# Optimization experiments

Hardware: AMD Instinct MI355X
Metric: run time of the kernel (lower is better)

Reference implementation:

```python
import jax, jax.numpy as jnp
import numpy as np

N_NODES = 50000
N_EDGES = 800000
D_IN = 128
D_HID = 128
NUM_LAYERS = 3
NUM_GRAPHS = 50


def setup_inputs() -> dict:
    key = jax.random.key(0)
    ks = jax.random.split(key, 8)
    x = jax.random.normal(ks[0], (N_NODES, D_IN), dtype=jnp.float32)
    edge_index = jax.random.randint(ks[1], (2, N_EDGES), 0, N_NODES, dtype=jnp.int32)
    batch = jnp.sort(jax.random.randint(ks[2], (N_NODES,), 0, NUM_GRAPHS, dtype=jnp.int32))
    # glorot-ish init for GCN weights and fc weights
    scale = 1.0 / np.sqrt(D_HID)
    Wc = jax.random.normal(ks[3], (NUM_LAYERS, D_IN, D_HID), dtype=jnp.float32) * scale
    bc = jnp.zeros((NUM_LAYERS, D_HID), dtype=jnp.float32)
    Wf = jax.random.normal(ks[4], (NUM_LAYERS, D_HID, D_HID), dtype=jnp.float32) * scale
    bf = jnp.zeros((NUM_LAYERS, D_HID), dtype=jnp.float32)
    return {"x": x, "edge_index": edge_index, "batch": batch,
            "Wc": Wc, "bc": bc, "Wf": Wf, "bf": bf}


def _gcn_forward(x, Wc, bc, Wf, bf, src, dst, deg_inv_sqrt, batch):
    norm = deg_inv_sqrt[src] * deg_inv_sqrt[dst]  # [E+N]
    for i in range(NUM_LAYERS):
        h = x @ Wc[i]                              # [N, D_HID] linear transform
        msg = h[src] * norm[:, None]               # gather + normalize, [E+N, D_HID]
        x = jax.ops.segment_sum(msg, dst, num_segments=N_NODES) + bc[i]
        x = jax.nn.relu(x)
    x = jax.ops.segment_sum(x, batch, num_segments=NUM_GRAPHS)  # global_add_pool
    for i in range(NUM_LAYERS):
        x = jax.nn.relu(x @ Wf[i] + bf[i])
    return x  # [NUM_GRAPHS, D_HID]


def reference(x, edge_index, batch, Wc, bc, Wf, bf):
    # add self-loops (PyG GCNConv default) and compute symmetric normalization
    loops = jnp.arange(N_NODES, dtype=edge_index.dtype)
    src = jnp.concatenate([edge_index[0], loops])
    dst = jnp.concatenate([edge_index[1], loops])
    deg = jax.ops.segment_sum(jnp.ones_like(dst, dtype=x.dtype), dst,
                              num_segments=N_NODES)
    deg_inv_sqrt = jnp.where(deg > 0, jax.lax.rsqrt(jnp.maximum(deg, 1.0)), 0.0)
    return _gcn_forward(x, Wc, bc, Wf, bf, src, dst, deg_inv_sqrt, batch)
```

## Files before the change

kernel.cpp:

```cpp
#include <hip/hip_runtime.h>

#define N_NODES 50000
#define N_EDGES 800000
#define D 128
#define NGRAPH 50

typedef unsigned int uint32;
typedef unsigned short u16;
typedef __attribute__((ext_vector_type(8))) short short8;
typedef __attribute__((ext_vector_type(4))) float f32x4;

__device__ inline float bf_lo(uint32 u) { union { uint32 u; float f; } c; c.u = u << 16; return c.f; }
__device__ inline float bf_hi(uint32 u) { union { uint32 u; float f; } c; c.u = u & 0xffff0000u; return c.f; }
__device__ inline u16 f2bf(float f) {
  union { float f; uint32 u; } c; c.f = f;
  uint32 r = (c.u + 0x7fffu + ((c.u >> 16) & 1u)) >> 16;
  return (u16)r;
}

__global__ void k_init(int* __restrict__ deg, const float* __restrict__ Wc,
                       u16* __restrict__ WT, const int* __restrict__ batch,
                       int* __restrict__ gstart) {
  int i = blockIdx.x * 256 + threadIdx.x;
  if (i < N_NODES) deg[i] = 0;
  if (i < 3 * 128 * 128) {
    int layer = i >> 14, rem = i & 16383;
    int n = rem >> 7, k = rem & 127;
    WT[i] = f2bf(Wc[layer * 16384 + k * 128 + n]);
  }
  if (i <= NGRAPH) {
    int lo = 0, hi = N_NODES;
    while (lo < hi) {
      int mid = (lo + hi) >> 1;
      if (batch[mid] < i) lo = mid + 1; else hi = mid;
    }
    gstart[i] = lo;
  }
}

__global__ void k_degfill(const int* __restrict__ src, const int* __restrict__ dst,
                          int* __restrict__ deg, u16* __restrict__ csr) {
  int part = blockIdx.x & 7;
  int e = (blockIdx.x >> 3) * 256 + threadIdx.x;
  if (e < N_EDGES) {
    int d = dst[e];
    if (d / 6250 == part) {
      int r = atomicAdd(&deg[d], 1);
      csr[(d << 6) + r] = (u16)src[e];
    }
  }
}

__global__ void k_prescale(const float4* __restrict__ x, const int* __restrict__ deg,
                           uint4* __restrict__ xs) {
  int i = blockIdx.x * 256 + threadIdx.x;
  if (i < N_NODES * 16) {
    int node = i >> 4;
    float di = rsqrtf((float)deg[node] + 1.0f);
    float4 v0 = x[(size_t)i * 2];
    float4 v1 = x[(size_t)i * 2 + 1];
    uint4 o;
    o.x = ((uint32)f2bf(di * v0.y) << 16) | f2bf(di * v0.x);
    o.y = ((uint32)f2bf(di * v0.w) << 16) | f2bf(di * v0.z);
    o.z = ((uint32)f2bf(di * v1.y) << 16) | f2bf(di * v1.x);
    o.w = ((uint32)f2bf(di * v1.w) << 16) | f2bf(di * v1.z);
    xs[i] = o;
  }
}

#define ACC8(A, u) do { \
    A##0 += bf_lo((u).x); A##1 += bf_hi((u).x); A##2 += bf_lo((u).y); A##3 += bf_hi((u).y); \
    A##4 += bf_lo((u).z); A##5 += bf_hi((u).z); A##6 += bf_lo((u).w); A##7 += bf_hi((u).w); } while (0)

#define RED2(v) do { v += __shfl_xor(v, 16); v += __shfl_xor(v, 32); } while (0)

template <int PRESCALE_OUT>
__global__ __launch_bounds__(256) void k_layer(const uint4* __restrict__ xs,
                                               const int* __restrict__ deg,
                                               const u16* __restrict__ csr,
                                               const u16* __restrict__ WT,
                                               const float* __restrict__ bc,
                                               u16* __restrict__ xo) {
  __shared__ u16 sa[4][16][136];
  int t = threadIdx.x;
  int wave = t >> 6, l = t & 63;
  int q = l >> 4, c = l & 15;
  int r0 = blockIdx.x * 64 + wave * 16;

  for (int n = 0; n < 16; n += 2) {
    int i0 = r0 + n, i1 = i0 + 1;
    bool v0 = i0 < N_NODES, v1 = i1 < N_NODES;
    int cntA = v0 ? deg[i0] : 0;
    int cntB = v1 ? deg[i1] : 0;

    float xA0 = 0.f, xA1 = 0.f, xA2 = 0.f, xA3 = 0.f, xA4 = 0.f, xA5 = 0.f, xA6 = 0.f, xA7 = 0.f;
    float xB0 = 0.f, xB1 = 0.f, xB2 = 0.f, xB3 = 0.f, xB4 = 0.f, xB5 = 0.f, xB6 = 0.f, xB7 = 0.f;

    if (q == 0 && v0) {
      uint4 su = xs[(size_t)i0 * 16 + c];
      ACC8(xA, su);
    } else if (q == 1 && v1) {
      uint4 su = xs[(size_t)i1 * 16 + c];
      ACC8(xB, su);
    }

    int myA = (l < cntA) ? (int)csr[(i0 << 6) + l] : 0;
    int myB = (l < cntB) ? (int)csr[(i1 << 6) + l] : 0;

    int nq = (max(cntA, cntB) + 3) >> 2;
#pragma unroll 4
    for (int j = 0; j < nq; ++j) {
      int idx = 4 * j + q;
      int sA = __shfl(myA, idx < cntA ? idx : 0);
      int sB = __shfl(myB, idx < cntB ? idx : 0);
      uint4 uA = xs[(size_t)sA * 16 + c];
      uint4 uB = xs[(size_t)sB * 16 + c];
      if (idx < cntA) ACC8(xA, uA);
      if (idx < cntB) ACC8(xB, uB);
    }

    RED2(xA0); RED2(xA1); RED2(xA2); RED2(xA3); RED2(xA4); RED2(xA5); RED2(xA6); RED2(xA7);
    RED2(xB0); RED2(xB1); RED2(xB2); RED2(xB3); RED2(xB4); RED2(xB5); RED2(xB6); RED2(xB7);

    if (q == 0) {
      uint4 o;
      o.x = ((uint32)f2bf(xA1) << 16) | f2bf(xA0);
      o.y = ((uint32)f2bf(xA3) << 16) | f2bf(xA2);
      o.z = ((uint32)f2bf(xA5) << 16) | f2bf(xA4);
      o.w = ((uint32)f2bf(xA7) << 16) | f2bf(xA6);
      *reinterpret_cast<uint4*>(&sa[wave][n][c * 8]) = o;
    } else if (q == 1) {
      uint4 o;
      o.x = ((uint32)f2bf(xB1) << 16) | f2bf(xB0);
      o.y = ((uint32)f2bf(xB3) << 16) | f2bf(xB2);
      o.z = ((uint32)f2bf(xB5) << 16) | f2bf(xB4);
      o.w = ((uint32)f2bf(xB7) << 16) | f2bf(xB6);
      *reinterpret_cast<uint4*>(&sa[wave][n + 1][c * 8]) = o;
    }
  }

  const short8* B8 = reinterpret_cast<const short8*>(WT);
  f32x4 acc[8] = {};
#pragma unroll
  for (int k0 = 0; k0 < 4; ++k0) {
    short8 a = *reinterpret_cast<const short8*>(&sa[wave][c][(k0 * 4 + q) * 8]);
#pragma unroll
    for (int cc = 0; cc < 8; ++cc) {
      short8 b = B8[(cc * 16 + c) * 16 + k0 * 4 + q];
      acc[cc] = __builtin_amdgcn_mfma_f32_16x16x32_bf16(a, b, acc[cc], 0, 0, 0);
    }
  }

  int rloc = q * 4;
  float dj[4];
#pragma unroll
  for (int j = 0; j < 4; ++j) {
    int rr = r0 + rloc + j;
    dj[j] = (rr < N_NODES) ? rsqrtf((float)deg[rr] + 1.0f) : 0.f;
  }
#pragma unroll
  for (int cc = 0; cc < 8; ++cc) {
    float bcv = bc[cc * 16 + c];
#pragma unroll
    for (int j = 0; j < 4; ++j) {
      float r = fmaxf(fmaf(dj[j], acc[cc][j], bcv), 0.f);
      if (PRESCALE_OUT) r *= dj[j];
      sa[wave][rloc + j][cc * 16 + c] = f2bf(r);
    }
  }

#pragma unroll
  for (int i = 0; i < 4; ++i) {
    int idx = i * 64 + l;
    int rr = idx >> 4, ch = idx & 15;
    int grow = r0 + rr;
    if (grow < N_NODES) {
      *reinterpret_cast<uint4*>(&xo[(size_t)grow * 128 + ch * 8]) =
          *reinterpret_cast<const uint4*>(&sa[wave][rr][ch * 8]);
    }
  }
}

__global__ __launch_bounds__(256) void k_pool(const uint32* __restrict__ xb,
                                              const int* __restrict__ gstart,
                                              float* __restrict__ pp) {
  __shared__ float2 red[4][64];
  int g = blockIdx.x, ch = blockIdx.y;
  int s = gstart[g], e = gstart[g + 1];
  long len = e - s;
  int cs = s + (int)(len * ch / 8);
  int ce = s + (int)(len * (ch + 1) / 8);
  int sub = threadIdx.x >> 6, l = threadIdx.x & 63;
  float2 acc = make_float2(0.f, 0.f);
  for (int n = cs + sub; n < ce; n += 4) {
    uint32 v = xb[(size_t)n * 64 + l];
    acc.x += bf_lo(v);
    acc.y += bf_hi(v);
  }
  red[sub][l] = acc;
  __syncthreads();
  if (sub == 0) {
    float2 a = red[0][l];
    a.x += red[1][l].x + red[2][l].x + red[3][l].x;
    a.y += red[1][l].y + red[2][l].y + red[3][l].y;
    pp[(ch * NGRAPH + g) * D + 2 * l] = a.x;
    pp[(ch * NGRAPH + g) * D + 2 * l + 1] = a.y;
  }
}

__global__ __launch_bounds__(128) void k_fc(const float* __restrict__ pp,
                                            const float* __restrict__ Wf,
                                            const float* __restrict__ bf,
                                            float* __restrict__ out) {
  __shared__ float row[D];
  int g = blockIdx.x, c = threadIdx.x;
  float v = 0.f;
#pragma unroll
  for (int ch = 0; ch < 8; ++ch) v += pp[(ch * NGRAPH + g) * D + c];
  row[c] = v;
  __syncthreads();
  for (int l = 0; l < 3; ++l) {
    const float* W = Wf + l * D * D;
    float s = bf[l * D + c];
    for (int k = 0; k < D; ++k) s = fmaf(row[k], W[k * D + c], s);
    s = fmaxf(s, 0.f);
    __syncthreads();
    row[c] = s;
    __syncthreads();
  }
  out[g * D + c] = row[c];
}

extern "C" void kernel_launch(void* const* d_in, const int* in_sizes, int n_in,
                              void* d_out, int out_size, void* d_ws, size_t ws_size,
                              hipStream_t stream) {
  const float* x   = (const float*)d_in[0];
  const int*   ei  = (const int*)d_in[1];
  const int* batch = (const int*)d_in[2];
  const float* Wc  = (const float*)d_in[3];
  const float* bc  = (const float*)d_in[4];
  const float* Wf  = (const float*)d_in[5];
  const float* bf  = (const float*)d_in[6];
  float* out = (float*)d_out;
  const int* src = ei;
  const int* dst = ei + N_EDGES;

  char* ws = (char*)d_ws;
  size_t o = 0;
  auto take = [&](size_t b) -> void* {
    void* p = ws + o;
    o = (o + b + 255) & ~(size_t)255;
    return p;
  };
  int*  deg    = (int*)take(N_NODES * 4);
  int*  gstart = (int*)take(64 * 4);
  u16*  WT     = (u16*)take((size_t)3 * D * D * 2);
  u16*  csr    = (u16*)take((size_t)N_NODES * 64 * 2);
  u16*  xsA    = (u16*)take((size_t)N_NODES * D * 2);
  u16*  xsB    = (u16*)take((size_t)N_NODES * D * 2);
  float* pp    = (float*)take((size_t)8 * NGRAPH * D * 4);
  (void)ws_size; (void)in_sizes; (void)n_in; (void)out_size;

  const int NB = (N_NODES + 255) / 256;
  k_init<<<NB, 256, 0, stream>>>(deg, Wc, WT, batch, gstart);
  k_degfill<<<8 * ((N_EDGES + 255) / 256), 256, 0, stream>>>(src, dst, deg, csr);
  k_prescale<<<(N_NODES * 16 + 255) / 256, 256, 0, stream>>>((const float4*)x, deg, (uint4*)xsA);

  const int GB = (N_NODES + 63) / 64;
  k_layer<1><<<GB, 256, 0, stream>>>((const uint4*)xsA, deg, csr, WT + 0 * D * D, bc + 0 * D, xsB);
  k_layer<1><<<GB, 256, 0, stream>>>((const uint4*)xsB, deg, csr, WT + 1 * D * D, bc + 1 * D, xsA);
  k_layer<0><<<GB, 256, 0, stream>>>((const uint4*)xsA, deg, csr, WT + 2 * D * D, bc + 2 * D, xsB);

  k_pool<<<dim3(NGRAPH, 8), 256, 0, stream>>>((const uint32*)xsB, gstart, pp);
  k_fc<<<NGRAPH, 128, 0, stream>>>(pp, Wf, bf, out);
}
```

Measured before the change: 232.5 us.

## Split each 16-row tile across four waves and share the MFMA output columns

Each block now handles 16 nodes instead of 64. Each wave gathers 4 nodes one at a time instead of 16 nodes in pairs, and the MFMA work is split so each wave computes 2 of the 8 output column tiles. Shared-memory tiles are shared across waves with barriers, the launch grid becomes four times larger, and bounds checks are dropped because N_NODES is divisible by 16. This cuts per-block serial gather work and raises the number of blocks for load balancing, at the cost of two __syncthreads per block and fewer independent loads in flight per wave.

```diff
diff --git a/kernel.cpp b/kernel.cpp
--- a/kernel.cpp
+++ b/kernel.cpp
@@ -81,104 +81,76 @@
                                                const u16* __restrict__ WT,
                                                const float* __restrict__ bc,
                                                u16* __restrict__ xo) {
-  __shared__ u16 sa[4][16][136];
+  __shared__ u16 sa[16][136];
+  __shared__ u16 so[16][136];
   int t = threadIdx.x;
   int wave = t >> 6, l = t & 63;
   int q = l >> 4, c = l & 15;
-  int r0 = blockIdx.x * 64 + wave * 16;
-
-  for (int n = 0; n < 16; n += 2) {
-    int i0 = r0 + n, i1 = i0 + 1;
-    bool v0 = i0 < N_NODES, v1 = i1 < N_NODES;
-    int cntA = v0 ? deg[i0] : 0;
-    int cntB = v1 ? deg[i1] : 0;
-
-    float xA0 = 0.f, xA1 = 0.f, xA2 = 0.f, xA3 = 0.f, xA4 = 0.f, xA5 = 0.f, xA6 = 0.f, xA7 = 0.f;
-    float xB0 = 0.f, xB1 = 0.f, xB2 = 0.f, xB3 = 0.f, xB4 = 0.f, xB5 = 0.f, xB6 = 0.f, xB7 = 0.f;
-
-    if (q == 0 && v0) {
-      uint4 su = xs[(size_t)i0 * 16 + c];
-      ACC8(xA, su);
-    } else if (q == 1 && v1) {
-      uint4 su = xs[(size_t)i1 * 16 + c];
-      ACC8(xB, su);
-    }
-
-    int myA = (l < cntA) ? (int)csr[(i0 << 6) + l] : 0;
-    int myB = (l < cntB) ? (int)csr[(i1 << 6) + l] : 0;
-
-    int nq = (max(cntA, cntB) + 3) >> 2;
+  int r0 = blockIdx.x * 16;
+
+  for (int n = 0; n < 4; ++n) {
+    int i = r0 + wave * 4 + n;
+    int cnt = deg[i];
+    float a0 = 0.f, a1 = 0.f, a2 = 0.f, a3 = 0.f, a4 = 0.f, a5 = 0.f, a6 = 0.f, a7 = 0.f;
+    if (q == 0) {
+      uint4 su = xs[(size_t)i * 16 + c];
+      ACC8(a, su);
+    }
+    int myidx = (l < cnt) ? (int)csr[(i << 6) + l] : 0;
+    int nq = (cnt + 3) >> 2;
 #pragma unroll 4
     for (int j = 0; j < nq; ++j) {
       int idx = 4 * j + q;
-      int sA = __shfl(myA, idx < cntA ? idx : 0);
-      int sB = __shfl(myB, idx < cntB ? idx : 0);
-      uint4 uA = xs[(size_t)sA * 16 + c];
-      uint4 uB = xs[(size_t)sB * 16 + c];
-      if (idx < cntA) ACC8(xA, uA);
-      if (idx < cntB) ACC8(xB, uB);
-    }
-
-    RED2(xA0); RED2(xA1); RED2(xA2); RED2(xA3); RED2(xA4); RED2(xA5); RED2(xA6); RED2(xA7);
-    RED2(xB0); RED2(xB1); RED2(xB2); RED2(xB3); RED2(xB4); RED2(xB5); RED2(xB6); RED2(xB7);
-
+      int s = __shfl(myidx, idx < cnt ? idx : 0);
+      uint4 u = xs[(size_t)s * 16 + c];
+      if (idx < cnt) ACC8(a, u);
+    }
+    RED2(a0); RED2(a1); RED2(a2); RED2(a3); RED2(a4); RED2(a5); RED2(a6); RED2(a7);
     if (q == 0) {
       uint4 o;
-      o.x = ((uint32)f2bf(xA1) << 16) | f2bf(xA0);
-      o.y = ((uint32)f2bf(xA3) << 16) | f2bf(xA2);
-      o.z = ((uint32)f2bf(xA5) << 16) | f2bf(xA4);
-      o.w = ((uint32)f2bf(xA7) << 16) | f2bf(xA6);
-      *reinterpret_cast<uint4*>(&sa[wave][n][c * 8]) = o;
-    } else if (q == 1) {
-      uint4 o;
-      o.x = ((uint32)f2bf(xB1) << 16) | f2bf(xB0);
-      o.y = ((uint32)f2bf(xB3) << 16) | f2bf(xB2);
-      o.z = ((uint32)f2bf(xB5) << 16) | f2bf(xB4);
-      o.w = ((uint32)f2bf(xB7) << 16) | f2bf(xB6);
-      *reinterpret_cast<uint4*>(&sa[wave][n + 1][c * 8]) = o;
-    }
-  }
+      o.x = ((uint32)f2bf(a1) << 16) | f2bf(a0);
+      o.y = ((uint32)f2bf(a3) << 16) | f2bf(a2);
+      o.z = ((uint32)f2bf(a5) << 16) | f2bf(a4);
+      o.w = ((uint32)f2bf(a7) << 16) | f2bf(a6);
+      *reinterpret_cast<uint4*>(&sa[wave * 4 + n][c * 8]) = o;
+    }
+  }
+  __syncthreads();
 
   const short8* B8 = reinterpret_cast<const short8*>(WT);
-  f32x4 acc[8] = {};
+  f32x4 acc[2] = {};
 #pragma unroll
   for (int k0 = 0; k0 < 4; ++k0) {
-    short8 a = *reinterpret_cast<const short8*>(&sa[wave][c][(k0 * 4 + q) * 8]);
-#pragma unroll
-    for (int cc = 0; cc < 8; ++cc) {
+    short8 a = *reinterpret_cast<const short8*>(&sa[c][(k0 * 4 + q) * 8]);
+#pragma unroll
+    for (int m = 0; m < 2; ++m) {
+      int cc = wave * 2 + m;
       short8 b = B8[(cc * 16 + c) * 16 + k0 * 4 + q];
-      acc[cc] = __builtin_amdgcn_mfma_f32_16x16x32_bf16(a, b, acc[cc], 0, 0, 0);
-    }
-  }
-
-  int rloc = q * 4;
+      acc[m] = __builtin_amdgcn_mfma_f32_16x16x32_bf16(a, b, acc[m], 0, 0, 0);
+    }
+  }
+
   float dj[4];
 #pragma unroll
   for (int j = 0; j < 4; ++j) {
-    int rr = r0 + rloc + j;
-    dj[j] = (rr < N_NODES) ? rsqrtf((float)deg[rr] + 1.0f) : 0.f;
-  }
-#pragma unroll
-  for (int cc = 0; cc < 8; ++cc) {
+    dj[j] = rsqrtf((float)deg[r0 + q * 4 + j] + 1.0f);
+  }
+#pragma unroll
+  for (int m = 0; m < 2; ++m) {
+    int cc = wave * 2 + m;
     float bcv = bc[cc * 16 + c];
 #pragma unroll
     for (int j = 0; j < 4; ++j) {
-      float r = fmaxf(fmaf(dj[j], acc[cc][j], bcv), 0.f);
+      float r = fmaxf(fmaf(dj[j], acc[m][j], bcv), 0.f);
       if (PRESCALE_OUT) r *= dj[j];
-      sa[wave][rloc + j][cc * 16 + c] = f2bf(r);
-    }
-  }
-
-#pragma unroll
-  for (int i = 0; i < 4; ++i) {
-    int idx = i * 64 + l;
-    int rr = idx >> 4, ch = idx & 15;
-    int grow = r0 + rr;
-    if (grow < N_NODES) {
-      *reinterpret_cast<uint4*>(&xo[(size_t)grow * 128 + ch * 8]) =
-          *reinterpret_cast<const uint4*>(&sa[wave][rr][ch * 8]);
-    }
-  }
+      so[q * 4 + j][cc * 16 + c] = f2bf(r);
+    }
+  }
+  __syncthreads();
+
+  int rr = t >> 4, ch = t & 15;
+  *reinterpret_cast<uint4*>(&xo[(size_t)(r0 + rr) * 128 + ch * 8]) =
+      *reinterpret_cast<const uint4*>(&so[rr][ch * 8]);
 }
 
 __global__ __launch_bounds__(256) void k_pool(const uint32* __restrict__ xb,
@@ -266,7 +238,7 @@
   k_degfill<<<8 * ((N_EDGES + 255) / 256), 256, 0, stream>>>(src, dst, deg, csr);
   k_prescale<<<(N_NODES * 16 + 255) / 256, 256, 0, stream>>>((const float4*)x, deg, (uint4*)xsA);
 
-  const int GB = (N_NODES + 63) / 64;
+  const int GB = N_NODES / 16;
   k_layer<1><<<GB, 256, 0, stream>>>((const uint4*)xsA, deg, csr, WT + 0 * D * D, bc + 0 * D, xsB);
   k_layer<1><<<GB, 256, 0, stream>>>((const uint4*)xsB, deg, csr, WT + 1 * D * D, bc + 1 * D, xsA);
   k_layer<0><<<GB, 256, 0, stream>>>((const uint4*)xsA, deg, csr, WT + 2 * D * D, bc + 2 * D, xsB);
```

Measured after the change: 204.4 us (median of 2 runs). 12.1% less time.
